# Optimization experiments

Hardware: AMD Instinct MI355X
Metric: run time of the kernel (lower is better)

The kernel has to match this reference:

```python
import jax, jax.numpy as jnp
import numpy as np

DIM = 512
HEADS = 8
HEAD = DIM // HEADS
T = 243          # temporal length, fixed by get_temporal_mask(243, ...)
N_JOINTS = 17    # skeleton joints
BATCH = 4        # number of clips; leading dim of x is BATCH*T
WINDOWS = (9, 27, 81, 243)  # temporal_MoE_type


def _temporal_masks():
    # Block-diagonal window masks: 0 inside each window block, -100000 outside,
    # exactly matching get_temporal_mask + torch.where(matrix == 0, -100000, 0).
    idx = np.arange(T)
    masks = np.stack([
        np.where((idx[:, None] // w) == (idx[None, :] // w), 0.0, -100000.0)
        for w in WINDOWS
    ]).astype(np.float32)  # (E, T, T)
    return jnp.asarray(masks)


def setup_inputs() -> dict:
    key = jax.random.key(0)
    k0, k1, k2, k3 = jax.random.split(key, 4)
    scaled = lambda k, shape, fan: jax.random.normal(k, shape, jnp.float32) * (fan ** -0.5)
    return {
        "x": jax.random.normal(k0, (BATCH * T, N_JOINTS, DIM), jnp.float32),
        "qkv_w": scaled(k1, (DIM, 3 * DIM), DIM),          # qkv (no bias, qkv_bias=False)
        "proj_w": scaled(k2, (DIM, DIM), DIM),             # output projection
        "proj_b": jnp.zeros((DIM,), jnp.float32),
        "te_w": scaled(k3, (DIM, len(WINDOWS)), DIM),      # temporal_expert_linear
        "te_b": jnp.zeros((len(WINDOWS),), jnp.float32),
        "seqlen": T,
    }


def reference(x, qkv_w, proj_w, proj_b, te_w, te_b, seqlen):
    BT, n, C = x.shape              # (b*T, N, C)
    b = BT // seqlen
    scale = HEAD ** -0.5
    # qkv projection -> q,k,v each (b, H, N, T, head_dim)
    qkv = (x @ qkv_w).reshape(b, seqlen, n, 3, HEADS, HEAD)
    qkv = jnp.transpose(qkv, (3, 0, 4, 2, 1, 5))  # (3, b, H, N, T, c)
    q, k, v = qkv[0], qkv[1], qkv[2]
    # temporal attention logits, shared across experts: (b, H, N, T, T)
    attn = jnp.einsum('bhntc,bhnsc->bhnts', q, k) * scale
    masks = _temporal_masks()                       # (E, T, T)
    attn = attn[None] + masks[:, None, None, None]  # (E, b, H, N, T, T)
    attn = jax.nn.softmax(attn, axis=-1)            # attn_drop is identity (p=0 / eval)
    eo = jnp.einsum('ebhnts,bhnsc->ebhntc', attn, v)
    E = masks.shape[0]
    # (E,b,H,N,T,c) -> (E,b,T,N,H,c) -> (E, b*T, N, C), matching permute(0,3,2,1,4)
    eo = jnp.transpose(eo, (0, 1, 4, 3, 2, 5)).reshape(E, BT, n, C)
    # expert gating: softmax(temporal_expert_linear(x)) over experts, per token
    w = jax.nn.softmax(x @ te_w + te_b, axis=-1)    # (BT, N, E)
    out = jnp.einsum('ebnc,bne->bnc', eo, w)        # fused expert recombination
    out = out @ proj_w + proj_b                     # proj (proj_drop identity)
    return out
```

## Files before the change

kernel.cpp:

```cpp
#include <hip/hip_runtime.h>
#include <hip/hip_bf16.h>
#include <cstdint>

#define TT 243
#define NJ 17
#define NB 4
#define NH 8
#define HD 64
#define CDIM 512
#define NROWS (NB*TT*NJ)
#define NBHN (NB*NH*NJ)

typedef unsigned short u16;
typedef __attribute__((ext_vector_type(8))) short short8;
typedef __attribute__((ext_vector_type(4))) float f32x4;

#define MFMA16(a, b, c) __builtin_amdgcn_mfma_f32_16x16x32_bf16((a), (b), (c), 0, 0, 0)
#define QSCALE 0.18033688011112042f

__device__ __forceinline__ void gl_lds16(const void* g, void* l) {
  __builtin_amdgcn_global_load_lds(
      (const __attribute__((address_space(1))) void*)g,
      (__attribute__((address_space(3))) void*)l, 16, 0, 0);
}

__device__ __forceinline__ u16 f2bf(float f) {
  union { float f; unsigned u; } v; v.f = f;
  unsigned r = v.u + 0x7FFFu + ((v.u >> 16) & 1u);
  return (u16)(r >> 16);
}

__device__ __forceinline__ float wave_reduce_sum(float v) {
#pragma unroll
  for (int off = 32; off > 0; off >>= 1) v += __shfl_xor(v, off, 64);
  return v;
}

__global__ __launch_bounds__(256) void convgates(
    const float* __restrict__ x, const float* __restrict__ te_w,
    const float* __restrict__ te_b, u16* __restrict__ xb,
    float* __restrict__ gates) {
  int w = threadIdx.x >> 6, l = threadIdx.x & 63;
  int row = blockIdx.x * 4 + w;
  if (row >= NROWS) return;
  const float* xr = x + (size_t)row * CDIM;
  u16* xo = xb + (size_t)row * CDIM;
  float a0 = 0.f, a1 = 0.f, a2 = 0.f, a3 = 0.f;
#pragma unroll
  for (int p = 0; p < 2; ++p) {
    int c = (p * 64 + l) * 4;
    float4 v = *(const float4*)(xr + c);
    ushort4 o;
    o.x = f2bf(v.x); o.y = f2bf(v.y); o.z = f2bf(v.z); o.w = f2bf(v.w);
    *(ushort4*)(xo + c) = o;
    float xv[4] = {v.x, v.y, v.z, v.w};
#pragma unroll
    for (int q = 0; q < 4; ++q) {
      float4 wv = *(const float4*)(te_w + (size_t)(c + q) * 4);
      a0 += xv[q] * wv.x; a1 += xv[q] * wv.y;
      a2 += xv[q] * wv.z; a3 += xv[q] * wv.w;
    }
  }
  a0 = wave_reduce_sum(a0);
  a1 = wave_reduce_sum(a1);
  a2 = wave_reduce_sum(a2);
  a3 = wave_reduce_sum(a3);
  a0 += te_b[0]; a1 += te_b[1]; a2 += te_b[2]; a3 += te_b[3];
  float mx = fmaxf(fmaxf(a0, a1), fmaxf(a2, a3));
  float e0 = __expf(a0 - mx), e1 = __expf(a1 - mx);
  float e2 = __expf(a2 - mx), e3 = __expf(a3 - mx);
  float inv = 1.f / (e0 + e1 + e2 + e3);
  if (l == 0) {
    *(float4*)(gates + (size_t)row * 4) =
        make_float4(e0 * inv, e1 * inv, e2 * inv, e3 * inv);
  }
}

__global__ __launch_bounds__(256) void trans_w(const float* __restrict__ in,
                                               u16* __restrict__ out, int K, int N) {
  __shared__ float tile[32][33];
  int n0 = blockIdx.x * 32, k0 = blockIdx.y * 32;
  int tx = threadIdx.x & 31, ty = threadIdx.x >> 5;
#pragma unroll
  for (int p = 0; p < 4; ++p)
    tile[ty + p * 8][tx] = in[(size_t)(k0 + ty + p * 8) * N + n0 + tx];
  __syncthreads();
#pragma unroll
  for (int p = 0; p < 4; ++p)
    out[(size_t)(n0 + ty + p * 8) * K + k0 + tx] = f2bf(tile[tx][ty + p * 8]);
}

__global__ __launch_bounds__(256) void qkv_gemm(
    const u16* __restrict__ xb, const u16* __restrict__ wt,
    u16* __restrict__ qh, u16* __restrict__ kh, u16* __restrict__ vb) {
  __shared__ u16 S[16640];
  u16* Al = S;
  u16* Bl = S + 8192;
  int tid = threadIdx.x;
  int w = tid >> 6, l = tid & 63;
  int c16 = tid & 15, g4 = (tid >> 4) & 3;
  int r0 = blockIdx.y * 128, n0 = blockIdx.x * 128;
  int wm = w & 1, wn = w >> 1;

  size_t arow[2]; int ac8[2], brow[2];
#pragma unroll
  for (int it = 0; it < 2; ++it) {
    int F = it * 256 + w * 64 + l;
    int row = F >> 2;
    ac8[it] = F & 3;
    brow[it] = n0 + row;
    int m = r0 + row; if (m >= NROWS) m = NROWS - 1;
    int bj = m / 243, t = m - bj * 243;
    int b = bj / 17, j = bj - b * 17;
    arow[it] = ((size_t)(b * 243 + t) * 17 + j) * 512;
  }

  f32x4 acc[4][4] = {};
  for (int k0 = 0; k0 < CDIM; k0 += 32) {
    __syncthreads();
#pragma unroll
    for (int it = 0; it < 2; ++it) {
      gl_lds16(xb + arow[it] + k0 + ac8[it] * 8,
               Al + (size_t)(it * 256 + w * 64) * 8);
      gl_lds16(wt + (size_t)brow[it] * 512 + k0 + ac8[it] * 8,
               Bl + (size_t)(it * 256 + w * 64) * 8);
    }
    __syncthreads();
    short8 af[4], bf[4];
#pragma unroll
    for (int i = 0; i < 4; ++i)
      af[i] = *(const short8*)(Al + ((wm * 64 + i * 16 + c16) * 32 + g4 * 8));
#pragma unroll
    for (int j = 0; j < 4; ++j)
      bf[j] = *(const short8*)(Bl + ((wn * 64 + j * 16 + c16) * 32 + g4 * 8));
#pragma unroll
    for (int i = 0; i < 4; ++i)
#pragma unroll
      for (int j = 0; j < 4; ++j)
        acc[i][j] = MFMA16(af[i], bf[j], acc[i][j]);
  }

  if (n0 < 1024) {
#pragma unroll
    for (int i = 0; i < 4; ++i)
#pragma unroll
      for (int r = 0; r < 4; ++r) {
        int m = r0 + wm * 64 + i * 16 + g4 * 4 + r;
        if (m >= NROWS) continue;
        int bj = m / 243, t = m - bj * 243;
        int b = bj / 17, j = bj - b * 17;
#pragma unroll
        for (int jt = 0; jt < 4; ++jt) {
          int col = n0 + wn * 64 + jt * 16 + c16;
          int sel = col >> 9, h = (col >> 6) & 7, c = col & 63;
          u16* dst = sel ? kh : qh;
          float val = acc[i][jt][r];
          if (!sel) val *= QSCALE;
          dst[((size_t)((b * 8 + h) * 17 + j) * 243 + t) * 64 + c] = f2bf(val);
        }
      }
  } else {
    __syncthreads();
#pragma unroll
    for (int i = 0; i < 4; ++i)
#pragma unroll
      for (int jt = 0; jt < 4; ++jt)
#pragma unroll
        for (int r = 0; r < 4; ++r) {
          int row = wm * 64 + i * 16 + g4 * 4 + r;
          int colI = wn * 64 + jt * 16 + c16;
          S[colI * 130 + row] = f2bf(acc[i][jt][r]);
        }
    __syncthreads();
    int hb = (n0 - 1024) >> 6;
    int m0 = r0 + 2 * l;
    int m1 = m0 + 1;
    bool v0 = m0 < NROWS, v1 = m1 < NROWS;
    int bj0 = m0 / 243, t0 = m0 - bj0 * 243;
    int b0 = bj0 / 17, j0 = bj0 - b0 * 17;
    int bj1 = m1 / 243, t1 = m1 - bj1 * 243;
    int b1 = bj1 / 17, j1 = bj1 - b1 * 17;
    size_t base0 = ((size_t)(b0 * 136 + j0) * 64) * 256 + t0;
    size_t base1 = ((size_t)(b1 * 136 + j1) * 64) * 256 + t1;
#pragma unroll 8
    for (int cc = 0; cc < 32; ++cc) {
      int colI = w * 32 + cc;
      int h = hb + (colI >> 6), c = colI & 63;
      ushort2 u = *(const ushort2*)&S[colI * 130 + 2 * l];
      size_t hoff = ((size_t)h * 17 * 64) * 256 + (size_t)c * 256;
      if (v0) vb[base0 + hoff] = u.x;
      if (v1) vb[base1 + hoff] = u.y;
    }
  }
}

__global__ __launch_bounds__(256, 4) void attn_kernel(
    const u16* __restrict__ qh, const u16* __restrict__ kh,
    const u16* __restrict__ vb, const float* __restrict__ gates,
    u16* __restrict__ preb) {
  __shared__ u16 L[16384];
  int bhn = blockIdx.x;
  int q0 = blockIdx.y * 64;
  int b = bhn / (NH * NJ);
  int hj = bhn - b * (NH * NJ);
  int h = hj / NJ, j = hj - h * NJ;
  int tid = threadIdx.x;
  int w = tid >> 6;
  int c16 = tid & 15, g4 = (tid >> 4) & 3;
  const u16* Kp = kh + (size_t)bhn * (TT * HD);
  const u16* Qp = qh + (size_t)bhn * (TT * HD);
  const u16* Vp = vb + (size_t)bhn * (HD * 256);
  u16* Rw = L + w * 4096;

#pragma unroll
  for (int it = 0; it < 8; ++it) {
    int F = it * 256 + tid;
    int s = F >> 3;
    int c8 = (F & 7) ^ (s & 7);
    int sg = s < TT ? s : TT - 1;
    gl_lds16(Kp + (size_t)sg * 64 + c8 * 8, L + (size_t)(it * 256 + (tid & ~63)) * 8);
  }
  __syncthreads();

  int tt = q0 + w * 16 + c16;
  bool tvalid = tt < TT;
  int tg = tvalid ? tt : TT - 1;

  short8 bq[2];
#pragma unroll
  for (int hh = 0; hh < 2; ++hh)
    bq[hh] = *(const short8*)(Qp + (size_t)tg * 64 + hh * 32 + g4 * 8);

  f32x4 acc[16];
#pragma unroll
  for (int st = 0; st < 16; ++st) acc[st] = (f32x4)(0.f);
#pragma unroll
  for (int st = 0; st < 16; ++st) {
    int sf = st * 16 + c16;
#pragma unroll
    for (int hh = 0; hh < 2; ++hh) {
      short8 ak = *(const short8*)(L + sf * 64 + ((hh * 4 + g4) ^ (sf & 7)) * 8);
      acc[st] = MFMA16(ak, bq[hh], acc[st]);
    }
  }
  __syncthreads();

  float M = -1e30f;
#pragma unroll
  for (int st = 0; st < 16; ++st)
#pragma unroll
    for (int r = 0; r < 4; ++r) {
      int s = st * 16 + g4 * 4 + r;
      float v = acc[st][r];
      v = (s < TT) ? v : -1e30f;
      acc[st][r] = v;
      M = fmaxf(M, v);
    }
  M = fmaxf(M, __shfl_xor(M, 16, 64));
  M = fmaxf(M, __shfl_xor(M, 32, 64));

#pragma unroll
  for (int st = 0; st < 16; ++st)
#pragma unroll
    for (int r = 0; r < 4; ++r) acc[st][r] = exp2f(acc[st][r] - M);

  int t9b = (tg / 9) * 9;
  int t27b = (tg / 27) * 27;
  int t81b = (tg / 81) * 81;
  float l9 = 0.f, l27 = 0.f, l81 = 0.f, l243 = 0.f;
#pragma unroll
  for (int st = 0; st < 16; ++st)
#pragma unroll
    for (int r = 0; r < 4; ++r) {
      int s = st * 16 + g4 * 4 + r;
      float e = acc[st][r];
      l243 += e;
      l81 += ((unsigned)(s - t81b) < 81u) ? e : 0.f;
      l27 += ((unsigned)(s - t27b) < 27u) ? e : 0.f;
      l9  += ((unsigned)(s - t9b)  <  9u) ? e : 0.f;
    }
  l9   += __shfl_xor(l9, 16, 64);   l9   += __shfl_xor(l9, 32, 64);
  l27  += __shfl_xor(l27, 16, 64);  l27  += __shfl_xor(l27, 32, 64);
  l81  += __shfl_xor(l81, 16, 64);  l81  += __shfl_xor(l81, 32, 64);
  l243 += __shfl_xor(l243, 16, 64); l243 += __shfl_xor(l243, 32, 64);

  float4 gv = *(const float4*)(gates + ((size_t)(b * TT + tg) * NJ + j) * 4);
  float gam3 = gv.w / l243;
  float gam2 = gam3 + gv.z / l81;
  float gam1 = gam2 + gv.y / l27;
  float gam0 = gam1 + gv.x / l9;

#pragma unroll
  for (int st = 0; st < 16; ++st) {
    float rv[4];
#pragma unroll
    for (int r = 0; r < 4; ++r) {
      int s = st * 16 + g4 * 4 + r;
      float e = acc[st][r];
      float cw = ((unsigned)(s - t9b) < 9u) ? gam0
               : ((unsigned)(s - t27b) < 27u) ? gam1
               : ((unsigned)(s - t81b) < 81u) ? gam2 : gam3;
      rv[r] = tvalid ? e * cw : 0.f;
    }
    uint2 pk;
    pk.x = (unsigned)f2bf(rv[0]) | ((unsigned)f2bf(rv[1]) << 16);
    pk.y = (unsigned)f2bf(rv[2]) | ((unsigned)f2bf(rv[3]) << 16);
    int c8 = st * 2 + (g4 >> 1);
    int slot = (c8 & 24) | ((c8 & 7) ^ (c16 & 7));
    *(uint2*)(Rw + c16 * 256 + slot * 8 + (g4 & 1) * 4) = pk;
  }

  short8 ar[8];
#pragma unroll
  for (int h2 = 0; h2 < 8; ++h2) {
    int cc = h2 * 4 + g4;
    int slot = (cc & 24) | ((cc & 7) ^ (c16 & 7));
    ar[h2] = *(const short8*)(Rw + c16 * 256 + slot * 8);
  }
#pragma unroll
  for (int jt = 0; jt < 4; ++jt) {
    int c = jt * 16 + c16;
    f32x4 o = (f32x4)(0.f);
#pragma unroll
    for (int h2 = 0; h2 < 8; ++h2) {
      short8 bv = *(const short8*)(Vp + (size_t)c * 256 + h2 * 32 + g4 * 8);
      o = MFMA16(ar[h2], bv, o);
    }
#pragma unroll
    for (int r = 0; r < 4; ++r) {
      int t = q0 + w * 16 + g4 * 4 + r;
      if (t < TT)
        preb[((size_t)(b * TT + t) * NJ + j) * 512 + h * 64 + c] = f2bf(o[r]);
    }
  }
}

__global__ __launch_bounds__(256) void proj_gemm(
    const u16* __restrict__ preb, const u16* __restrict__ pwt,
    const float* __restrict__ bias, float* __restrict__ out) {
  __shared__ u16 Al[128 * 32];
  __shared__ u16 Bl[128 * 32];
  int tid = threadIdx.x;
  int w = tid >> 6, l = tid & 63;
  int c16 = tid & 15, g4 = (tid >> 4) & 3;
  int r0 = blockIdx.y * 128, n0 = blockIdx.x * 128;
  int wm = w & 1, wn = w >> 1;
  f32x4 acc[4][4] = {};
  for (int k0 = 0; k0 < CDIM; k0 += 32) {
    __syncthreads();
#pragma unroll
    for (int it = 0; it < 2; ++it) {
      int F = it * 256 + w * 64 + l;
      int row = F >> 2, c8 = F & 3;
      int gr = r0 + row; gr = gr < NROWS ? gr : NROWS - 1;
      gl_lds16(preb + (size_t)gr * 512 + k0 + c8 * 8,
               Al + (size_t)(it * 256 + w * 64) * 8);
      gl_lds16(pwt + (size_t)(n0 + row) * 512 + k0 + c8 * 8,
               Bl + (size_t)(it * 256 + w * 64) * 8);
    }
    __syncthreads();
    short8 af[4], bf[4];
#pragma unroll
    for (int i = 0; i < 4; ++i)
      af[i] = *(const short8*)(Al + ((wm * 64 + i * 16 + c16) * 32 + g4 * 8));
#pragma unroll
    for (int j = 0; j < 4; ++j)
      bf[j] = *(const short8*)(Bl + ((wn * 64 + j * 16 + c16) * 32 + g4 * 8));
#pragma unroll
    for (int i = 0; i < 4; ++i)
#pragma unroll
      for (int j = 0; j < 4; ++j)
        acc[i][j] = MFMA16(af[i], bf[j], acc[i][j]);
  }
#pragma unroll
  for (int i = 0; i < 4; ++i)
#pragma unroll
    for (int r = 0; r < 4; ++r) {
      int row = r0 + wm * 64 + i * 16 + g4 * 4 + r;
      if (row >= NROWS) continue;
#pragma unroll
      for (int jt = 0; jt < 4; ++jt) {
        int col = n0 + wn * 64 + jt * 16 + c16;
        out[(size_t)row * 512 + col] = acc[i][jt][r] + bias[col];
      }
    }
}

extern "C" void kernel_launch(void* const* d_in, const int* in_sizes, int n_in,
                              void* d_out, int out_size, void* d_ws, size_t ws_size,
                              hipStream_t stream) {
  (void)in_sizes; (void)n_in; (void)out_size; (void)ws_size;
  const float* x      = (const float*)d_in[0];
  const float* qkv_w  = (const float*)d_in[1];
  const float* proj_w = (const float*)d_in[2];
  const float* proj_b = (const float*)d_in[3];
  const float* te_w   = (const float*)d_in[4];
  const float* te_b   = (const float*)d_in[5];

  char* p = (char*)d_ws;
  auto alloc = [&](size_t bytes) {
    void* r = (void*)p;
    p += (bytes + 255) & ~(size_t)255;
    return r;
  };
  u16*   xb    = (u16*)alloc((size_t)NROWS * 512 * 2);
  u16*   wt    = (u16*)alloc((size_t)1536 * 512 * 2);
  u16*   pwt   = (u16*)alloc((size_t)512 * 512 * 2);
  float* gates = (float*)alloc((size_t)NROWS * 4 * 4);
  u16*   qhb   = (u16*)alloc((size_t)NBHN * 243 * 64 * 2);
  u16*   khb   = (u16*)alloc((size_t)NBHN * 243 * 64 * 2);
  u16*   vb    = (u16*)alloc((size_t)NBHN * 64 * 256 * 2);
  u16*   preb  = (u16*)alloc((size_t)NROWS * 512 * 2);
  float* out   = (float*)d_out;

  hipLaunchKernelGGL(convgates, dim3((NROWS + 3) / 4), dim3(256), 0, stream,
                     x, te_w, te_b, xb, gates);
  hipLaunchKernelGGL(trans_w, dim3(48, 16), dim3(256), 0, stream,
                     qkv_w, wt, 512, 1536);
  hipLaunchKernelGGL(trans_w, dim3(16, 16), dim3(256), 0, stream,
                     proj_w, pwt, 512, 512);
  hipLaunchKernelGGL(qkv_gemm, dim3(12, (NROWS + 127) / 128), dim3(256), 0, stream,
                     xb, wt, qhb, khb, vb);
  hipLaunchKernelGGL(attn_kernel, dim3(NBHN, 4), dim3(256), 0, stream,
                     qhb, khb, vb, gates, preb);
  hipLaunchKernelGGL(proj_gemm, dim3(4, (NROWS + 127) / 128), dim3(256), 0, stream,
                     preb, pwt, proj_b, out);
}
```

Measured before the change: 233.7 us.

## Merge prep kernels, deepen GEMM K-tiles with swizzled LDS, use fast intrinsics

Three preprocessing launches (bf16 conversion with gating, and two weight transposes) become one prep kernel that picks its job by block index, saving launch gaps. Both GEMMs now load 64-wide K tiles into an XOR-swizzled LDS layout, which halves the number of barrier pairs per tile and should cut LDS bank conflicts. The attention softmax masks padding only in the last tile and uses hardware exp2 and reciprocal, and bf16 packing switches to a packed-convert intrinsic. This trades a little precision in the reciprocal and exp2 approximations and doubles the LDS footprint of proj_gemm.

```diff
diff --git a/kernel.cpp b/kernel.cpp
--- a/kernel.cpp
+++ b/kernel.cpp
@@ -30,18 +30,74 @@
   return (u16)(r >> 16);
 }
 
+__device__ __forceinline__ float fast_exp2(float x) {
+#if __has_builtin(__builtin_amdgcn_exp2f)
+  return __builtin_amdgcn_exp2f(x);
+#else
+  return exp2f(x);
+#endif
+}
+__device__ __forceinline__ float fast_rcp(float x) {
+#if __has_builtin(__builtin_amdgcn_rcpf)
+  return __builtin_amdgcn_rcpf(x);
+#else
+  return 1.f / x;
+#endif
+}
+__device__ __forceinline__ unsigned pk_bf16(float a, float b) {
+#if __has_builtin(__builtin_amdgcn_cvt_pk_bf16_f32)
+  auto pk = __builtin_amdgcn_cvt_pk_bf16_f32(a, b);
+  unsigned u; __builtin_memcpy(&u, &pk, sizeof(u));
+  return u;
+#else
+  return (unsigned)f2bf(a) | ((unsigned)f2bf(b) << 16);
+#endif
+}
+
 __device__ __forceinline__ float wave_reduce_sum(float v) {
 #pragma unroll
   for (int off = 32; off > 0; off >>= 1) v += __shfl_xor(v, off, 64);
   return v;
 }
 
-__global__ __launch_bounds__(256) void convgates(
+#define CG_BLOCKS ((NROWS + 3) / 4)
+#define T1_NB 48
+#define T1_BLOCKS (48 * 16)
+#define T2_NB 16
+#define T2_BLOCKS (16 * 16)
+
+__device__ __forceinline__ void trans_body(const float* __restrict__ in,
+                                           u16* __restrict__ out, int K, int N,
+                                           int nb, int kb, float (*tile)[33]) {
+  int n0 = nb * 32, k0 = kb * 32;
+  int tx = threadIdx.x & 31, ty = threadIdx.x >> 5;
+#pragma unroll
+  for (int p = 0; p < 4; ++p)
+    tile[ty + p * 8][tx] = in[(size_t)(k0 + ty + p * 8) * N + n0 + tx];
+  __syncthreads();
+#pragma unroll
+  for (int p = 0; p < 4; ++p)
+    out[(size_t)(n0 + ty + p * 8) * K + k0 + tx] = f2bf(tile[tx][ty + p * 8]);
+}
+
+__global__ __launch_bounds__(256) void prep_kernel(
     const float* __restrict__ x, const float* __restrict__ te_w,
-    const float* __restrict__ te_b, u16* __restrict__ xb,
-    float* __restrict__ gates) {
+    const float* __restrict__ te_b, const float* __restrict__ qkv_w,
+    const float* __restrict__ proj_w, u16* __restrict__ xb,
+    float* __restrict__ gates, u16* __restrict__ wt, u16* __restrict__ pwt) {
+  __shared__ float tile[32][33];
+  int bid = blockIdx.x;
+  if (bid >= CG_BLOCKS) {
+    int r = bid - CG_BLOCKS;
+    if (r < T1_BLOCKS) trans_body(qkv_w, wt, 512, 1536, r % T1_NB, r / T1_NB, tile);
+    else {
+      r -= T1_BLOCKS;
+      trans_body(proj_w, pwt, 512, 512, r % T2_NB, r / T2_NB, tile);
+    }
+    return;
+  }
   int w = threadIdx.x >> 6, l = threadIdx.x & 63;
-  int row = blockIdx.x * 4 + w;
+  int row = bid * 4 + w;
   if (row >= NROWS) return;
   const float* xr = x + (size_t)row * CDIM;
   u16* xo = xb + (size_t)row * CDIM;
@@ -50,9 +106,10 @@
   for (int p = 0; p < 2; ++p) {
     int c = (p * 64 + l) * 4;
     float4 v = *(const float4*)(xr + c);
-    ushort4 o;
-    o.x = f2bf(v.x); o.y = f2bf(v.y); o.z = f2bf(v.z); o.w = f2bf(v.w);
-    *(ushort4*)(xo + c) = o;
+    uint2 o;
+    o.x = pk_bf16(v.x, v.y);
+    o.y = pk_bf16(v.z, v.w);
+    *(uint2*)(xo + c) = o;
     float xv[4] = {v.x, v.y, v.z, v.w};
 #pragma unroll
     for (int q = 0; q < 4; ++q) {
@@ -69,25 +126,11 @@
   float mx = fmaxf(fmaxf(a0, a1), fmaxf(a2, a3));
   float e0 = __expf(a0 - mx), e1 = __expf(a1 - mx);
   float e2 = __expf(a2 - mx), e3 = __expf(a3 - mx);
-  float inv = 1.f / (e0 + e1 + e2 + e3);
+  float inv = fast_rcp(e0 + e1 + e2 + e3);
   if (l == 0) {
     *(float4*)(gates + (size_t)row * 4) =
         make_float4(e0 * inv, e1 * inv, e2 * inv, e3 * inv);
   }
-}
-
-__global__ __launch_bounds__(256) void trans_w(const float* __restrict__ in,
-                                               u16* __restrict__ out, int K, int N) {
-  __shared__ float tile[32][33];
-  int n0 = blockIdx.x * 32, k0 = blockIdx.y * 32;
-  int tx = threadIdx.x & 31, ty = threadIdx.x >> 5;
-#pragma unroll
-  for (int p = 0; p < 4; ++p)
-    tile[ty + p * 8][tx] = in[(size_t)(k0 + ty + p * 8) * N + n0 + tx];
-  __syncthreads();
-#pragma unroll
-  for (int p = 0; p < 4; ++p)
-    out[(size_t)(n0 + ty + p * 8) * K + k0 + tx] = f2bf(tile[tx][ty + p * 8]);
 }
 
 __global__ __launch_bounds__(256) void qkv_gemm(
@@ -97,47 +140,55 @@
   u16* Al = S;
   u16* Bl = S + 8192;
   int tid = threadIdx.x;
-  int w = tid >> 6, l = tid & 63;
+  int w = tid >> 6;
   int c16 = tid & 15, g4 = (tid >> 4) & 3;
   int r0 = blockIdx.y * 128, n0 = blockIdx.x * 128;
   int wm = w & 1, wn = w >> 1;
 
-  size_t arow[2]; int ac8[2], brow[2];
-#pragma unroll
-  for (int it = 0; it < 2; ++it) {
-    int F = it * 256 + w * 64 + l;
-    int row = F >> 2;
-    ac8[it] = F & 3;
-    brow[it] = n0 + row;
-    int m = r0 + row; if (m >= NROWS) m = NROWS - 1;
+  int rA = tid >> 3;
+  int c8off = (((tid & 7) ^ (rA & 7)) * 8);
+  size_t arow4[4], brow4[4];
+#pragma unroll
+  for (int it = 0; it < 4; ++it) {
+    int m = r0 + it * 32 + rA;
+    if (m >= NROWS) m = NROWS - 1;
     int bj = m / 243, t = m - bj * 243;
     int b = bj / 17, j = bj - b * 17;
-    arow[it] = ((size_t)(b * 243 + t) * 17 + j) * 512;
+    arow4[it] = ((size_t)(b * 243 + t) * 17 + j) * 512;
+    brow4[it] = (size_t)(n0 + it * 32 + rA) * 512;
   }
 
   f32x4 acc[4][4] = {};
-  for (int k0 = 0; k0 < CDIM; k0 += 32) {
-    __syncthreads();
-#pragma unroll
-    for (int it = 0; it < 2; ++it) {
-      gl_lds16(xb + arow[it] + k0 + ac8[it] * 8,
-               Al + (size_t)(it * 256 + w * 64) * 8);
-      gl_lds16(wt + (size_t)brow[it] * 512 + k0 + ac8[it] * 8,
-               Bl + (size_t)(it * 256 + w * 64) * 8);
-    }
-    __syncthreads();
-    short8 af[4], bf[4];
+  for (int k0 = 0; k0 < CDIM; k0 += 64) {
+    __syncthreads();
+#pragma unroll
+    for (int it = 0; it < 4; ++it) {
+      gl_lds16(xb + arow4[it] + k0 + c8off, Al + (size_t)(it * 256 + (w * 64)) * 8);
+      gl_lds16(wt + brow4[it] + k0 + c8off, Bl + (size_t)(it * 256 + (w * 64)) * 8);
+    }
+    __syncthreads();
+    short8 af[4][2], bf[4][2];
+#pragma unroll
+    for (int i = 0; i < 4; ++i) {
+      int rowa = wm * 64 + i * 16 + c16;
+#pragma unroll
+      for (int hh = 0; hh < 2; ++hh)
+        af[i][hh] = *(const short8*)(Al + rowa * 64 + (((hh * 4 + g4) ^ (c16 & 7)) * 8));
+    }
+#pragma unroll
+    for (int j = 0; j < 4; ++j) {
+      int rowb = wn * 64 + j * 16 + c16;
+#pragma unroll
+      for (int hh = 0; hh < 2; ++hh)
+        bf[j][hh] = *(const short8*)(Bl + rowb * 64 + (((hh * 4 + g4) ^ (c16 & 7)) * 8));
+    }
 #pragma unroll
     for (int i = 0; i < 4; ++i)
-      af[i] = *(const short8*)(Al + ((wm * 64 + i * 16 + c16) * 32 + g4 * 8));
-#pragma unroll
-    for (int j = 0; j < 4; ++j)
-      bf[j] = *(const short8*)(Bl + ((wn * 64 + j * 16 + c16) * 32 + g4 * 8));
-#pragma unroll
-    for (int i = 0; i < 4; ++i)
-#pragma unroll
-      for (int j = 0; j < 4; ++j)
-        acc[i][j] = MFMA16(af[i], bf[j], acc[i][j]);
+#pragma unroll
+      for (int j = 0; j < 4; ++j) {
+        acc[i][j] = MFMA16(af[i][0], bf[j][0], acc[i][j]);
+        acc[i][j] = MFMA16(af[i][1], bf[j][1], acc[i][j]);
+      }
   }
 
   if (n0 < 1024) {
@@ -172,6 +223,7 @@
           S[colI * 130 + row] = f2bf(acc[i][jt][r]);
         }
     __syncthreads();
+    int l = tid & 63;
     int hb = (n0 - 1024) >> 6;
     int m0 = r0 + 2 * l;
     int m1 = m0 + 1;
@@ -245,24 +297,23 @@
   }
   __syncthreads();
 
+#pragma unroll
+  for (int r = 0; r < 4; ++r) {
+    int s = 240 + g4 * 4 + r;
+    if (s >= TT) acc[15][r] = -1e30f;
+  }
   float M = -1e30f;
 #pragma unroll
   for (int st = 0; st < 16; ++st)
 #pragma unroll
-    for (int r = 0; r < 4; ++r) {
-      int s = st * 16 + g4 * 4 + r;
-      float v = acc[st][r];
-      v = (s < TT) ? v : -1e30f;
-      acc[st][r] = v;
-      M = fmaxf(M, v);
-    }
+    for (int r = 0; r < 4; ++r) M = fmaxf(M, acc[st][r]);
   M = fmaxf(M, __shfl_xor(M, 16, 64));
   M = fmaxf(M, __shfl_xor(M, 32, 64));
 
 #pragma unroll
   for (int st = 0; st < 16; ++st)
 #pragma unroll
-    for (int r = 0; r < 4; ++r) acc[st][r] = exp2f(acc[st][r] - M);
+    for (int r = 0; r < 4; ++r) acc[st][r] = fast_exp2(acc[st][r] - M);
 
   int t9b = (tg / 9) * 9;
   int t27b = (tg / 27) * 27;
@@ -285,10 +336,10 @@
   l243 += __shfl_xor(l243, 16, 64); l243 += __shfl_xor(l243, 32, 64);
 
   float4 gv = *(const float4*)(gates + ((size_t)(b * TT + tg) * NJ + j) * 4);
-  float gam3 = gv.w / l243;
-  float gam2 = gam3 + gv.z / l81;
-  float gam1 = gam2 + gv.y / l27;
-  float gam0 = gam1 + gv.x / l9;
+  float gam3 = gv.w * fast_rcp(l243);
+  float gam2 = gam3 + gv.z * fast_rcp(l81);
+  float gam1 = gam2 + gv.y * fast_rcp(l27);
+  float gam0 = gam1 + gv.x * fast_rcp(l9);
 
 #pragma unroll
   for (int st = 0; st < 16; ++st) {
@@ -303,8 +354,8 @@
       rv[r] = tvalid ? e * cw : 0.f;
     }
     uint2 pk;
-    pk.x = (unsigned)f2bf(rv[0]) | ((unsigned)f2bf(rv[1]) << 16);
-    pk.y = (unsigned)f2bf(rv[2]) | ((unsigned)f2bf(rv[3]) << 16);
+    pk.x = pk_bf16(rv[0], rv[1]);
+    pk.y = pk_bf16(rv[2], rv[3]);
     int c8 = st * 2 + (g4 >> 1);
     int slot = (c8 & 24) | ((c8 & 7) ^ (c16 & 7));
     *(uint2*)(Rw + c16 * 256 + slot * 8 + (g4 & 1) * 4) = pk;
@@ -338,39 +389,56 @@
 __global__ __launch_bounds__(256) void proj_gemm(
     const u16* __restrict__ preb, const u16* __restrict__ pwt,
     const float* __restrict__ bias, float* __restrict__ out) {
-  __shared__ u16 Al[128 * 32];
-  __shared__ u16 Bl[128 * 32];
+  __shared__ u16 Al[8192];
+  __shared__ u16 Bl[8192];
   int tid = threadIdx.x;
-  int w = tid >> 6, l = tid & 63;
+  int w = tid >> 6;
   int c16 = tid & 15, g4 = (tid >> 4) & 3;
   int r0 = blockIdx.y * 128, n0 = blockIdx.x * 128;
   int wm = w & 1, wn = w >> 1;
+
+  int rA = tid >> 3;
+  int c8off = (((tid & 7) ^ (rA & 7)) * 8);
+  size_t arow4[4], brow4[4];
+#pragma unroll
+  for (int it = 0; it < 4; ++it) {
+    int m = r0 + it * 32 + rA;
+    if (m >= NROWS) m = NROWS - 1;
+    arow4[it] = (size_t)m * 512;
+    brow4[it] = (size_t)(n0 + it * 32 + rA) * 512;
+  }
+
   f32x4 acc[4][4] = {};
-  for (int k0 = 0; k0 < CDIM; k0 += 32) {
-    __syncthreads();
-#pragma unroll
-    for (int it = 0; it < 2; ++it) {
-      int F = it * 256 + w * 64 + l;
-      int row = F >> 2, c8 = F & 3;
-      int gr = r0 + row; gr = gr < NROWS ? gr : NROWS - 1;
-      gl_lds16(preb + (size_t)gr * 512 + k0 + c8 * 8,
-               Al + (size_t)(it * 256 + w * 64) * 8);
-      gl_lds16(pwt + (size_t)(n0 + row) * 512 + k0 + c8 * 8,
-               Bl + (size_t)(it * 256 + w * 64) * 8);
-    }
-    __syncthreads();
-    short8 af[4], bf[4];
+  for (int k0 = 0; k0 < CDIM; k0 += 64) {
+    __syncthreads();
+#pragma unroll
+    for (int it = 0; it < 4; ++it) {
+      gl_lds16(preb + arow4[it] + k0 + c8off, Al + (size_t)(it * 256 + (w * 64)) * 8);
+      gl_lds16(pwt + brow4[it] + k0 + c8off, Bl + (size_t)(it * 256 + (w * 64)) * 8);
+    }
+    __syncthreads();
+    short8 af[4][2], bf[4][2];
+#pragma unroll
+    for (int i = 0; i < 4; ++i) {
+      int rowa = wm * 64 + i * 16 + c16;
+#pragma unroll
+      for (int hh = 0; hh < 2; ++hh)
+        af[i][hh] = *(const short8*)(Al + rowa * 64 + (((hh * 4 + g4) ^ (c16 & 7)) * 8));
+    }
+#pragma unroll
+    for (int j = 0; j < 4; ++j) {
+      int rowb = wn * 64 + j * 16 + c16;
+#pragma unroll
+      for (int hh = 0; hh < 2; ++hh)
+        bf[j][hh] = *(const short8*)(Bl + rowb * 64 + (((hh * 4 + g4) ^ (c16 & 7)) * 8));
+    }
 #pragma unroll
     for (int i = 0; i < 4; ++i)
-      af[i] = *(const short8*)(Al + ((wm * 64 + i * 16 + c16) * 32 + g4 * 8));
-#pragma unroll
-    for (int j = 0; j < 4; ++j)
-      bf[j] = *(const short8*)(Bl + ((wn * 64 + j * 16 + c16) * 32 + g4 * 8));
-#pragma unroll
-    for (int i = 0; i < 4; ++i)
-#pragma unroll
-      for (int j = 0; j < 4; ++j)
-        acc[i][j] = MFMA16(af[i], bf[j], acc[i][j]);
+#pragma unroll
+      for (int j = 0; j < 4; ++j) {
+        acc[i][j] = MFMA16(af[i][0], bf[j][0], acc[i][j]);
+        acc[i][j] = MFMA16(af[i][1], bf[j][1], acc[i][j]);
+      }
   }
 #pragma unroll
   for (int i = 0; i < 4; ++i)
@@ -413,12 +481,8 @@
   u16*   preb  = (u16*)alloc((size_t)NROWS * 512 * 2);
   float* out   = (float*)d_out;
 
-  hipLaunchKernelGGL(convgates, dim3((NROWS + 3) / 4), dim3(256), 0, stream,
-                     x, te_w, te_b, xb, gates);
-  hipLaunchKernelGGL(trans_w, dim3(48, 16), dim3(256), 0, stream,
-                     qkv_w, wt, 512, 1536);
-  hipLaunchKernelGGL(trans_w, dim3(16, 16), dim3(256), 0, stream,
-                     proj_w, pwt, 512, 512);
+  hipLaunchKernelGGL(prep_kernel, dim3(CG_BLOCKS + T1_BLOCKS + T2_BLOCKS), dim3(256),
+                     0, stream, x, te_w, te_b, qkv_w, proj_w, xb, gates, wt, pwt);
   hipLaunchKernelGGL(qkv_gemm, dim3(12, (NROWS + 127) / 128), dim3(256), 0, stream,
                      xb, wt, qhb, khb, vb);
   hipLaunchKernelGGL(attn_kernel, dim3(NBHN, 4), dim3(256), 0, stream,
```

Measured after the change: 213.5 us. -8.7%, faster.
